# Optimization experiments

Measured on AMD Instinct MI355X. Metric: run time of the kernel, lower is better.

## Reference

```python
import jax, jax.numpy as jnp
import numpy as np

B, S, D = 1, 2048, 2048
H, KV = 32, 8
HD = D // H          # 64
R = H // KV          # 4 (GQA repeat factor)
ROPE_BASE = 10000.0


def setup_inputs() -> dict:
    key = jax.random.key(0)
    ks = jax.random.split(key, 5)
    x = jax.random.normal(ks[0], (B, S, D), jnp.float32)
    # Real rotary frequencies as (cos, sin) pairs: [S, HD//2, 2]
    inv_freq = 1.0 / (ROPE_BASE ** (np.arange(0, HD, 2, dtype=np.float64) / HD))
    ang = np.outer(np.arange(S, dtype=np.float64), inv_freq)
    freqs_cis = jnp.asarray(np.stack([np.cos(ang), np.sin(ang)], axis=-1), jnp.float32)
    std = 0.02
    wq = jax.random.normal(ks[1], (H * HD, D), jnp.float32) * std
    wk = jax.random.normal(ks[2], (KV * HD, D), jnp.float32) * std
    wv = jax.random.normal(ks[3], (KV * HD, D), jnp.float32) * std
    wo = jax.random.normal(ks[4], (D, H * HD), jnp.float32) * std
    return {"x": x, "freqs_cis": freqs_cis, "wq": wq, "wk": wk, "wv": wv, "wo": wo}


def _apply_rope(x, cos, sin):
    # x: [b, s, h, hd]; cos/sin: [s, hd//2]. Complex multiply on interleaved pairs.
    xr = x.reshape(*x.shape[:-1], HD // 2, 2)
    x0, x1 = xr[..., 0], xr[..., 1]
    c = cos[None, :, None, :]
    s = sin[None, :, None, :]
    o0 = x0 * c - x1 * s
    o1 = x0 * s + x1 * c
    return jnp.stack([o0, o1], axis=-1).reshape(x.shape)


def reference(x, freqs_cis, wq, wk, wv, wo):
    b, s, _ = x.shape
    q = (x @ wq.T).reshape(b, s, H, HD)
    k = (x @ wk.T).reshape(b, s, KV, HD)
    v = (x @ wv.T).reshape(b, s, KV, HD)
    cos, sin = freqs_cis[..., 0], freqs_cis[..., 1]
    q = _apply_rope(q, cos, sin)
    k = _apply_rope(k, cos, sin)
    # GQA: group q heads instead of repeat_interleave on k/v.
    # repeat_interleave maps kv-head g -> q heads [g*R, (g+1)*R), matching this reshape.
    qg = q.reshape(b, s, KV, R, HD)
    scale = 1.0 / np.sqrt(HD)
    scores = jnp.einsum('bsgrd,btgd->bgrst', qg, k) * scale  # [b, KV, R, s, t]
    causal = jnp.tril(jnp.ones((s, s), dtype=bool))
    scores = jnp.where(causal, scores, jnp.float32(-1e9))
    attn = jax.nn.softmax(scores.astype(jnp.float32), axis=-1).astype(q.dtype)
    out = jnp.einsum('bgrst,btgd->bsgrd', attn, v).reshape(b, s, H * HD)
    return out @ wo.T
```

## Files before the change

### kernel.cpp

```cpp
#include <hip/hip_runtime.h>

typedef unsigned short u16;
typedef unsigned int u32;
typedef __bf16 bf16x8 __attribute__((ext_vector_type(8)));
typedef unsigned short ushort8 __attribute__((ext_vector_type(8)));
typedef float floatx4 __attribute__((ext_vector_type(4)));
typedef u32 u32x2 __attribute__((ext_vector_type(2)));

#define S_LEN 2048
#define NH 32
#define NKV 8
#define HD_ 64
#define LDQ 3072

__device__ __forceinline__ u16 f2bf(float f) {
  unsigned u = __builtin_bit_cast(unsigned, f);
  u += 0x7FFF + ((u >> 16) & 1);
  return (u16)(u >> 16);
}
__device__ __forceinline__ float bf2f(u16 h) {
  unsigned u = ((unsigned)h) << 16;
  return __builtin_bit_cast(float, u);
}
__device__ __forceinline__ bf16x8 ld8(const u16* p) {
  return __builtin_bit_cast(bf16x8, *(const ushort8*)p);
}
__device__ __forceinline__ floatx4 mfma16(bf16x8 a, bf16x8 b, floatx4 c) {
  return __builtin_amdgcn_mfma_f32_16x16x32_bf16(a, b, c, 0, 0, 0);
}
__device__ __forceinline__ u32 pk2bf(float a, float b) {
  u32 ua = __builtin_bit_cast(u32, a) + 0x8000u;
  u32 ub = __builtin_bit_cast(u32, b) + 0x8000u;
  return __builtin_amdgcn_perm(ub, ua, 0x07060302);
}

__global__ void cvt_kernel(const float* __restrict__ in, u16* __restrict__ out, int n4) {
  int i = blockIdx.x * blockDim.x + threadIdx.x;
  if (i >= n4) return;
  float4 v = ((const float4*)in)[i];
  ((ushort4*)out)[i] = make_ushort4(f2bf(v.x), f2bf(v.y), f2bf(v.z), f2bf(v.w));
}

template <int TM, int TN, int OUT_BF16>
__global__ __launch_bounds__(256) void gemm_db(
    const u16* __restrict__ A, const u16* __restrict__ B, void* __restrict__ C,
    int ldc, int K, int lda) {
  __shared__ __align__(16) u16 As[2][TM * 64];
  __shared__ __align__(16) u16 Bs[2][TN * 64];
  const int tid = threadIdx.x;
  const int wave = tid >> 6, lane = tid & 63;
  const int quad = lane >> 4, l16 = lane & 15;
  const int bm = blockIdx.y * TM, bn = blockIdx.x * TN;
  const int wr = (wave >> 1) * (TM / 2), wc = (wave & 1) * (TN / 2);
  constexpr int MI = TM / 32, NI = TN / 32;
  const int crow = tid >> 3, col8 = tid & 7;

  size_t aoff[MI], boff[NI];
#pragma unroll
  for (int j = 0; j < MI; j++) aoff[j] = (size_t)(bm + crow + j * 32) * lda + col8 * 8;
#pragma unroll
  for (int j = 0; j < NI; j++) boff[j] = (size_t)(bn + crow + j * 32) * K + col8 * 8;

  ushort8 a8[MI], b8[NI];
  auto load_tiles = [&](int k0) {
#pragma unroll
    for (int j = 0; j < MI; j++) a8[j] = *(const ushort8*)(A + aoff[j] + k0);
#pragma unroll
    for (int j = 0; j < NI; j++) b8[j] = *(const ushort8*)(B + boff[j] + k0);
  };
  auto write_tiles = [&](int p) {
#pragma unroll
    for (int j = 0; j < MI; j++) {
      const int row = crow + j * 32;
      *(ushort8*)&As[p][row * 64 + ((col8 ^ (row & 7)) * 8)] = a8[j];
    }
#pragma unroll
    for (int j = 0; j < NI; j++) {
      const int row = crow + j * 32;
      *(ushort8*)&Bs[p][row * 64 + ((col8 ^ (row & 7)) * 8)] = b8[j];
    }
  };

  floatx4 acc[MI][NI] = {};
  load_tiles(0);
  write_tiles(0);
  __syncthreads();
  int p = 0;
  for (int k0 = 0; k0 < K; k0 += 64) {
    const bool more = (k0 + 64 < K);
    if (more) load_tiles(k0 + 64);
#pragma unroll
    for (int kh = 0; kh < 2; kh++) {
      bf16x8 af[MI], bfr[NI];
#pragma unroll
      for (int mi = 0; mi < MI; mi++) {
        const int row = wr + mi * 16 + l16;
        af[mi] = ld8(&As[p][row * 64 + (((kh * 4 + quad) ^ (row & 7)) * 8)]);
      }
#pragma unroll
      for (int ni = 0; ni < NI; ni++) {
        const int row = wc + ni * 16 + l16;
        bfr[ni] = ld8(&Bs[p][row * 64 + (((kh * 4 + quad) ^ (row & 7)) * 8)]);
      }
#pragma unroll
      for (int mi = 0; mi < MI; mi++)
#pragma unroll
        for (int ni = 0; ni < NI; ni++)
          acc[mi][ni] = mfma16(af[mi], bfr[ni], acc[mi][ni]);
    }
    if (more) {
      write_tiles(p ^ 1);
      __syncthreads();
      p ^= 1;
    }
  }

#pragma unroll
  for (int mi = 0; mi < MI; mi++)
#pragma unroll
    for (int ni = 0; ni < NI; ni++)
#pragma unroll
      for (int r = 0; r < 4; r++) {
        const int row = bm + wr + mi * 16 + quad * 4 + r;
        const int col = bn + wc + ni * 16 + l16;
        if (OUT_BF16) ((u16*)C)[(size_t)row * ldc + col] = f2bf(acc[mi][ni][r]);
        else          ((float*)C)[(size_t)row * ldc + col] = acc[mi][ni][r];
      }
}

__global__ void rope_kernel(u16* __restrict__ qk, const float* __restrict__ fc, int h_bits,
                            int row_stride, float scale) {
  int idx = blockIdx.x * blockDim.x + threadIdx.x;
  int d = idx & 31;
  int t = idx >> 5;
  int hh = t & ((1 << h_bits) - 1);
  int s = t >> h_bits;
  float c  = fc[s * 64 + d * 2];
  float sn = fc[s * 64 + d * 2 + 1];
  size_t base = (size_t)s * row_stride + hh * 64 + d * 2;
  float x0 = bf2f(qk[base]), x1 = bf2f(qk[base + 1]);
  qk[base]     = f2bf((x0 * c - x1 * sn) * scale);
  qk[base + 1] = f2bf((x0 * sn + x1 * c) * scale);
}

__global__ void transpose_v(const u16* __restrict__ qkv, u16* __restrict__ vT) {
  int idx = blockIdx.x * blockDim.x + threadIdx.x;
  int s = idx & (S_LEN - 1);
  int t = idx >> 11;
  vT[idx] = qkv[(size_t)s * LDQ + 2560 + t];
}

__global__ __launch_bounds__(256) void attn_kernel(const u16* qkv, const u16* __restrict__ vT,
                                                   u16* __restrict__ o) {
  __shared__ __align__(16) u16 Ks[64 * 72];
  __shared__ __align__(16) u16 Vs[64 * 72];
  __shared__ __align__(16) u16 pS[4][16 * 72];
  const int h = blockIdx.x;
  const int g = h >> 2;
  const int tid = threadIdx.x;
  const int wave = tid >> 6, lane = tid & 63;
  const int quad = lane >> 4, l16 = lane & 15;
  const int qtA = (int)blockIdx.y;
  const int qtB = 31 - qtA;

  const ushort8 ones_u = {0x3F80, 0x3F80, 0x3F80, 0x3F80, 0x3F80, 0x3F80, 0x3F80, 0x3F80};
  const bf16x8 onesA = __builtin_bit_cast(bf16x8, ones_u);

  const int qrow = wave * 16 + l16;
  const size_t qoffA = (size_t)(qtA * 64 + qrow) * LDQ + h * HD_;
  const size_t qoffB = (size_t)(qtB * 64 + qrow) * LDQ + h * HD_;
  bf16x8 qfA0 = ld8(qkv + qoffA + quad * 8);
  bf16x8 qfA1 = ld8(qkv + qoffA + 32 + quad * 8);
  bf16x8 qfB0 = ld8(qkv + qoffB + quad * 8);
  bf16x8 qfB1 = ld8(qkv + qoffB + 32 + quad * 8);

  const int r0 = tid >> 3,         o0 = (tid & 7) * 8;
  const int r1 = (tid + 256) >> 3, o1 = o0;
  const u16* ksrc = qkv + 2048 + g * HD_;
  const u16* vsrc = vT + (size_t)g * HD_ * S_LEN;

  ushort8 kp0 = *(const ushort8*)(ksrc + (size_t)r0 * LDQ + o0);
  ushort8 kp1 = *(const ushort8*)(ksrc + (size_t)r1 * LDQ + o1);
  ushort8 vp0 = *(const ushort8*)(vsrc + (size_t)r0 * S_LEN + o0);
  ushort8 vp1 = *(const ushort8*)(vsrc + (size_t)r1 * S_LEN + o1);

  u16* myP = &pS[wave][0];

  for (int ph = 0; ph < 2; ph++) {
    const int qt = ph ? qtB : qtA;
    const int qglob = qt * 64 + qrow;
    const bf16x8 qf0 = ph ? qfB0 : qfA0;
    const bf16x8 qf1 = ph ? qfB1 : qfA1;
    floatx4 Ofrag[4] = {};
    floatx4 lacc = {};

    for (int kt = 0; kt <= qt; kt++) {
      const int kbase = kt * 64;
      *(ushort8*)&Ks[r0 * 72 + o0] = kp0;
      *(ushort8*)&Ks[r1 * 72 + o1] = kp1;
      *(ushort8*)&Vs[r0 * 72 + o0] = vp0;
      *(ushort8*)&Vs[r1 * 72 + o1] = vp1;
      __syncthreads();
      const bool last = (kt == qt);
      if (!last || ph == 0) {
        const int nb = last ? 0 : kbase + 64;
        kp0 = *(const ushort8*)(ksrc + (size_t)(nb + r0) * LDQ + o0);
        kp1 = *(const ushort8*)(ksrc + (size_t)(nb + r1) * LDQ + o1);
        vp0 = *(const ushort8*)(vsrc + (size_t)r0 * S_LEN + nb + o0);
        vp1 = *(const ushort8*)(vsrc + (size_t)r1 * S_LEN + nb + o1);
      }
      floatx4 sf[4];
#pragma unroll
      for (int sub = 0; sub < 4; sub++) {
        const u16* kb = &Ks[(sub * 16 + l16) * 72];
        floatx4 s = {};
        s = mfma16(ld8(kb + quad * 8), qf0, s);
        s = mfma16(ld8(kb + 32 + quad * 8), qf1, s);
        sf[sub] = s;
      }
      if (last) {
#pragma unroll
        for (int sub = 0; sub < 4; sub++)
#pragma unroll
          for (int r = 0; r < 4; r++)
            if (kbase + sub * 16 + quad * 4 + r > qglob) sf[sub][r] = -INFINITY;
      }
      u32x2 pk[4];
#pragma unroll
      for (int sub = 0; sub < 4; sub++) {
        float p0 = __builtin_amdgcn_exp2f(sf[sub][0]);
        float p1 = __builtin_amdgcn_exp2f(sf[sub][1]);
        float p2 = __builtin_amdgcn_exp2f(sf[sub][2]);
        float p3 = __builtin_amdgcn_exp2f(sf[sub][3]);
        pk[sub].x = pk2bf(p0, p1);
        pk[sub].y = pk2bf(p2, p3);
      }
      bf16x8 vf[4][2];
#pragma unroll
      for (int nt = 0; nt < 4; nt++) {
        const u16* vb = &Vs[(nt * 16 + l16) * 72 + quad * 8];
        vf[nt][0] = ld8(vb);
        vf[nt][1] = ld8(vb + 32);
      }
#pragma unroll
      for (int sub = 0; sub < 4; sub++)
        *(u32x2*)&myP[l16 * 72 + sub * 16 + quad * 4] = pk[sub];
      asm volatile("s_waitcnt lgkmcnt(0)" ::: "memory");
      bf16x8 pf0 = ld8(&myP[l16 * 72 + quad * 8]);
      bf16x8 pf1 = ld8(&myP[l16 * 72 + 32 + quad * 8]);
#pragma unroll
      for (int nt = 0; nt < 4; nt++) {
        Ofrag[nt] = mfma16(vf[nt][0], pf0, Ofrag[nt]);
        Ofrag[nt] = mfma16(vf[nt][1], pf1, Ofrag[nt]);
      }
      lacc = mfma16(onesA, pf0, lacc);
      lacc = mfma16(onesA, pf1, lacc);
      __syncthreads();
    }

    const float inv = 1.0f / lacc[0];
    const size_t ooff = (size_t)qglob * 2048 + h * HD_;
#pragma unroll
    for (int nt = 0; nt < 4; nt++)
#pragma unroll
      for (int r = 0; r < 4; r++) {
        int hd = nt * 16 + quad * 4 + r;
        o[ooff + hd] = f2bf(Ofrag[nt][r] * inv);
      }
  }
}

extern "C" void kernel_launch(void* const* d_in, const int* in_sizes, int n_in,
                              void* d_out, int out_size, void* d_ws, size_t ws_size,
                              hipStream_t stream) {
  const float* x  = (const float*)d_in[0];
  const float* fc = (const float*)d_in[1];
  const float* wq = (const float*)d_in[2];
  const float* wk = (const float*)d_in[3];
  const float* wv = (const float*)d_in[4];
  const float* wo = (const float*)d_in[5];
  float* out = (float*)d_out;

  char* ws = (char*)d_ws;
  const size_t MB = 1024 * 1024;
  u16* qkv = (u16*)(ws);
  u16* wb  = (u16*)(ws + 12 * MB);
  u16* vTb = (u16*)(ws + 12 * MB);
  u16* wob = (u16*)(ws + 14 * MB);
  u16* ob  = (u16*)(ws + 22 * MB);
  u16* xb  = (u16*)d_out;
  (void)ws_size; (void)n_in; (void)in_sizes; (void)out_size;

  cvt_kernel<<<4096, 256, 0, stream>>>(x,  xb, 1048576);
  cvt_kernel<<<4096, 256, 0, stream>>>(wq, wb, 1048576);
  cvt_kernel<<<1024, 256, 0, stream>>>(wk, wb + (size_t)2048 * 2048, 262144);
  cvt_kernel<<<1024, 256, 0, stream>>>(wv, wb + (size_t)2560 * 2048, 262144);
  gemm_db<128, 96, 1><<<dim3(32, 16), 256, 0, stream>>>(xb, wb, qkv, LDQ, 2048, 2048);
  cvt_kernel<<<4096, 256, 0, stream>>>(wo, wob, 1048576);
  rope_kernel<<<8192, 256, 0, stream>>>(qkv, fc, 5, LDQ, 0.18033688f);
  rope_kernel<<<2048, 256, 0, stream>>>(qkv + 2048, fc, 3, LDQ, 1.0f);
  transpose_v<<<4096, 256, 0, stream>>>(qkv, vTb);
  attn_kernel<<<dim3(NH, 16), 256, 0, stream>>>(qkv, vTb, ob);
  gemm_db<128, 64, 0><<<dim3(32, 16), 256, 0, stream>>>(ob, wob, out, 2048, 2048, 2048);
}
```

Baseline: 233.8 us.

## Share K/V tiles across paired query tiles with double-buffered swizzled LDS

The attention kernel now processes its low and high causal query tiles together in one sweep over key tiles. Each K/V tile loaded into shared memory serves both query tiles, where before each of the two phases reloaded it. Shared memory is double-buffered, so the next tile is stored before compute and only one barrier runs per iteration. Row padding is replaced by an XOR swizzle. This cuts global and LDS traffic and synchronisation, at the cost of more registers for two sets of accumulators and divergent actA branches.

Result: no change. 231.8 us (-0.9%).

```diff
diff --git a/kernel.cpp b/kernel.cpp
--- a/kernel.cpp
+++ b/kernel.cpp
@@ -152,122 +152,176 @@
 
 __global__ __launch_bounds__(256) void attn_kernel(const u16* qkv, const u16* __restrict__ vT,
                                                    u16* __restrict__ o) {
-  __shared__ __align__(16) u16 Ks[64 * 72];
-  __shared__ __align__(16) u16 Vs[64 * 72];
-  __shared__ __align__(16) u16 pS[4][16 * 72];
+  __shared__ __align__(16) u16 Ks[2][64 * 64];
+  __shared__ __align__(16) u16 Vs[2][64 * 64];
+  __shared__ __align__(16) u16 pS[8][16 * 64];
   const int h = blockIdx.x;
   const int g = h >> 2;
   const int tid = threadIdx.x;
   const int wave = tid >> 6, lane = tid & 63;
   const int quad = lane >> 4, l16 = lane & 15;
-  const int qtA = (int)blockIdx.y;
-  const int qtB = 31 - qtA;
+  const int y = (int)blockIdx.y;
+  const int p_ = (y < 8) ? y : 23 - y;
+  const int qlo = p_, qhi = 31 - p_;
 
   const ushort8 ones_u = {0x3F80, 0x3F80, 0x3F80, 0x3F80, 0x3F80, 0x3F80, 0x3F80, 0x3F80};
   const bf16x8 onesA = __builtin_bit_cast(bf16x8, ones_u);
 
   const int qrow = wave * 16 + l16;
-  const size_t qoffA = (size_t)(qtA * 64 + qrow) * LDQ + h * HD_;
-  const size_t qoffB = (size_t)(qtB * 64 + qrow) * LDQ + h * HD_;
+  const int qgA = qlo * 64 + qrow, qgB = qhi * 64 + qrow;
+  const size_t qoffA = (size_t)qgA * LDQ + h * HD_;
+  const size_t qoffB = (size_t)qgB * LDQ + h * HD_;
   bf16x8 qfA0 = ld8(qkv + qoffA + quad * 8);
   bf16x8 qfA1 = ld8(qkv + qoffA + 32 + quad * 8);
   bf16x8 qfB0 = ld8(qkv + qoffB + quad * 8);
   bf16x8 qfB1 = ld8(qkv + qoffB + 32 + quad * 8);
 
-  const int r0 = tid >> 3,         o0 = (tid & 7) * 8;
-  const int r1 = (tid + 256) >> 3, o1 = o0;
+  const int r0 = tid >> 3, r1 = r0 + 32;
+  const int col8 = tid & 7;
+  const int so = (col8 ^ (r0 & 7)) * 8;
+  const int o0 = col8 * 8;
   const u16* ksrc = qkv + 2048 + g * HD_;
   const u16* vsrc = vT + (size_t)g * HD_ * S_LEN;
 
   ushort8 kp0 = *(const ushort8*)(ksrc + (size_t)r0 * LDQ + o0);
-  ushort8 kp1 = *(const ushort8*)(ksrc + (size_t)r1 * LDQ + o1);
+  ushort8 kp1 = *(const ushort8*)(ksrc + (size_t)r1 * LDQ + o0);
   ushort8 vp0 = *(const ushort8*)(vsrc + (size_t)r0 * S_LEN + o0);
-  ushort8 vp1 = *(const ushort8*)(vsrc + (size_t)r1 * S_LEN + o1);
-
-  u16* myP = &pS[wave][0];
-
-  for (int ph = 0; ph < 2; ph++) {
-    const int qt = ph ? qtB : qtA;
-    const int qglob = qt * 64 + qrow;
-    const bf16x8 qf0 = ph ? qfB0 : qfA0;
-    const bf16x8 qf1 = ph ? qfB1 : qfA1;
-    floatx4 Ofrag[4] = {};
-    floatx4 lacc = {};
-
-    for (int kt = 0; kt <= qt; kt++) {
-      const int kbase = kt * 64;
-      *(ushort8*)&Ks[r0 * 72 + o0] = kp0;
-      *(ushort8*)&Ks[r1 * 72 + o1] = kp1;
-      *(ushort8*)&Vs[r0 * 72 + o0] = vp0;
-      *(ushort8*)&Vs[r1 * 72 + o1] = vp1;
+  ushort8 vp1 = *(const ushort8*)(vsrc + (size_t)r1 * S_LEN + o0);
+
+  floatx4 OA[4] = {}, OB[4] = {};
+  floatx4 lA = {}, lB = {};
+  u16* myPA = &pS[wave][0];
+  u16* myPB = &pS[wave + 4][0];
+
+  *(ushort8*)&Ks[0][r0 * 64 + so] = kp0;
+  *(ushort8*)&Ks[0][r1 * 64 + so] = kp1;
+  *(ushort8*)&Vs[0][r0 * 64 + so] = vp0;
+  *(ushort8*)&Vs[0][r1 * 64 + so] = vp1;
+  kp0 = *(const ushort8*)(ksrc + (size_t)(64 + r0) * LDQ + o0);
+  kp1 = *(const ushort8*)(ksrc + (size_t)(64 + r1) * LDQ + o0);
+  vp0 = *(const ushort8*)(vsrc + (size_t)r0 * S_LEN + 64 + o0);
+  vp1 = *(const ushort8*)(vsrc + (size_t)r1 * S_LEN + 64 + o0);
+  __syncthreads();
+  int pp = 0;
+
+  for (int kt = 0; kt <= qhi; kt++) {
+    const int kbase = kt * 64;
+    const bool more = kt < qhi;
+    if (more) {
+      *(ushort8*)&Ks[pp ^ 1][r0 * 64 + so] = kp0;
+      *(ushort8*)&Ks[pp ^ 1][r1 * 64 + so] = kp1;
+      *(ushort8*)&Vs[pp ^ 1][r0 * 64 + so] = vp0;
+      *(ushort8*)&Vs[pp ^ 1][r1 * 64 + so] = vp1;
+      if (kt + 1 < qhi) {
+        const int nb = kbase + 128;
+        kp0 = *(const ushort8*)(ksrc + (size_t)(nb + r0) * LDQ + o0);
+        kp1 = *(const ushort8*)(ksrc + (size_t)(nb + r1) * LDQ + o0);
+        vp0 = *(const ushort8*)(vsrc + (size_t)r0 * S_LEN + nb + o0);
+        vp1 = *(const ushort8*)(vsrc + (size_t)r1 * S_LEN + nb + o0);
+      }
+    }
+    const u16* Kc = &Ks[pp][0];
+    const u16* Vc = &Vs[pp][0];
+    const bool actA = (kt <= qlo);
+
+    floatx4 sfA[4], sfB[4];
+#pragma unroll
+    for (int sub = 0; sub < 4; sub++) {
+      const int row = sub * 16 + l16;
+      const u16* kb = Kc + row * 64;
+      bf16x8 k0 = ld8(kb + ((quad ^ (l16 & 7)) * 8));
+      bf16x8 k1 = ld8(kb + (((4 + quad) ^ (l16 & 7)) * 8));
+      floatx4 sB = {};
+      sB = mfma16(k0, qfB0, sB);
+      sB = mfma16(k1, qfB1, sB);
+      sfB[sub] = sB;
+      if (actA) {
+        floatx4 sA = {};
+        sA = mfma16(k0, qfA0, sA);
+        sA = mfma16(k1, qfA1, sA);
+        sfA[sub] = sA;
+      }
+    }
+    if (kt == qhi) {
+#pragma unroll
+      for (int sub = 0; sub < 4; sub++)
+#pragma unroll
+        for (int r = 0; r < 4; r++)
+          if (kbase + sub * 16 + quad * 4 + r > qgB) sfB[sub][r] = -INFINITY;
+    }
+    if (kt == qlo) {
+#pragma unroll
+      for (int sub = 0; sub < 4; sub++)
+#pragma unroll
+        for (int r = 0; r < 4; r++)
+          if (kbase + sub * 16 + quad * 4 + r > qgA) sfA[sub][r] = -INFINITY;
+    }
+
+    u32x2 pkA[4], pkB[4];
+#pragma unroll
+    for (int sub = 0; sub < 4; sub++) {
+      pkB[sub].x = pk2bf(__builtin_amdgcn_exp2f(sfB[sub][0]), __builtin_amdgcn_exp2f(sfB[sub][1]));
+      pkB[sub].y = pk2bf(__builtin_amdgcn_exp2f(sfB[sub][2]), __builtin_amdgcn_exp2f(sfB[sub][3]));
+      if (actA) {
+        pkA[sub].x = pk2bf(__builtin_amdgcn_exp2f(sfA[sub][0]), __builtin_amdgcn_exp2f(sfA[sub][1]));
+        pkA[sub].y = pk2bf(__builtin_amdgcn_exp2f(sfA[sub][2]), __builtin_amdgcn_exp2f(sfA[sub][3]));
+      }
+    }
+
+    bf16x8 vf[4][2];
+#pragma unroll
+    for (int nt = 0; nt < 4; nt++) {
+      const u16* vb = Vc + (nt * 16 + l16) * 64;
+      vf[nt][0] = ld8(vb + ((quad ^ (l16 & 7)) * 8));
+      vf[nt][1] = ld8(vb + (((4 + quad) ^ (l16 & 7)) * 8));
+    }
+
+#pragma unroll
+    for (int sub = 0; sub < 4; sub++) {
+      const int slot = (2 * sub + (quad >> 1)) ^ (l16 & 7);
+      const int a = l16 * 64 + slot * 8 + (quad & 1) * 4;
+      *(u32x2*)&myPB[a] = pkB[sub];
+      if (actA) *(u32x2*)&myPA[a] = pkA[sub];
+    }
+    asm volatile("s_waitcnt lgkmcnt(0)" ::: "memory");
+    bf16x8 pB0 = ld8(&myPB[l16 * 64 + ((quad ^ (l16 & 7)) * 8)]);
+    bf16x8 pB1 = ld8(&myPB[l16 * 64 + (((4 + quad) ^ (l16 & 7)) * 8)]);
+#pragma unroll
+    for (int nt = 0; nt < 4; nt++) {
+      OB[nt] = mfma16(vf[nt][0], pB0, OB[nt]);
+      OB[nt] = mfma16(vf[nt][1], pB1, OB[nt]);
+    }
+    lB = mfma16(onesA, pB0, lB);
+    lB = mfma16(onesA, pB1, lB);
+    if (actA) {
+      bf16x8 pA0 = ld8(&myPA[l16 * 64 + ((quad ^ (l16 & 7)) * 8)]);
+      bf16x8 pA1 = ld8(&myPA[l16 * 64 + (((4 + quad) ^ (l16 & 7)) * 8)]);
+#pragma unroll
+      for (int nt = 0; nt < 4; nt++) {
+        OA[nt] = mfma16(vf[nt][0], pA0, OA[nt]);
+        OA[nt] = mfma16(vf[nt][1], pA1, OA[nt]);
+      }
+      lA = mfma16(onesA, pA0, lA);
+      lA = mfma16(onesA, pA1, lA);
+    }
+    if (more) {
       __syncthreads();
-      const bool last = (kt == qt);
-      if (!last || ph == 0) {
-        const int nb = last ? 0 : kbase + 64;
-        kp0 = *(const ushort8*)(ksrc + (size_t)(nb + r0) * LDQ + o0);
-        kp1 = *(const ushort8*)(ksrc + (size_t)(nb + r1) * LDQ + o1);
-        vp0 = *(const ushort8*)(vsrc + (size_t)r0 * S_LEN + nb + o0);
-        vp1 = *(const ushort8*)(vsrc + (size_t)r1 * S_LEN + nb + o1);
-      }
-      floatx4 sf[4];
-#pragma unroll
-      for (int sub = 0; sub < 4; sub++) {
-        const u16* kb = &Ks[(sub * 16 + l16) * 72];
-        floatx4 s = {};
-        s = mfma16(ld8(kb + quad * 8), qf0, s);
-        s = mfma16(ld8(kb + 32 + quad * 8), qf1, s);
-        sf[sub] = s;
-      }
-      if (last) {
-#pragma unroll
-        for (int sub = 0; sub < 4; sub++)
-#pragma unroll
-          for (int r = 0; r < 4; r++)
-            if (kbase + sub * 16 + quad * 4 + r > qglob) sf[sub][r] = -INFINITY;
-      }
-      u32x2 pk[4];
-#pragma unroll
-      for (int sub = 0; sub < 4; sub++) {
-        float p0 = __builtin_amdgcn_exp2f(sf[sub][0]);
-        float p1 = __builtin_amdgcn_exp2f(sf[sub][1]);
-        float p2 = __builtin_amdgcn_exp2f(sf[sub][2]);
-        float p3 = __builtin_amdgcn_exp2f(sf[sub][3]);
-        pk[sub].x = pk2bf(p0, p1);
-        pk[sub].y = pk2bf(p2, p3);
-      }
-      bf16x8 vf[4][2];
-#pragma unroll
-      for (int nt = 0; nt < 4; nt++) {
-        const u16* vb = &Vs[(nt * 16 + l16) * 72 + quad * 8];
-        vf[nt][0] = ld8(vb);
-        vf[nt][1] = ld8(vb + 32);
-      }
-#pragma unroll
-      for (int sub = 0; sub < 4; sub++)
-        *(u32x2*)&myP[l16 * 72 + sub * 16 + quad * 4] = pk[sub];
-      asm volatile("s_waitcnt lgkmcnt(0)" ::: "memory");
-      bf16x8 pf0 = ld8(&myP[l16 * 72 + quad * 8]);
-      bf16x8 pf1 = ld8(&myP[l16 * 72 + 32 + quad * 8]);
-#pragma unroll
-      for (int nt = 0; nt < 4; nt++) {
-        Ofrag[nt] = mfma16(vf[nt][0], pf0, Ofrag[nt]);
-        Ofrag[nt] = mfma16(vf[nt][1], pf1, Ofrag[nt]);
-      }
-      lacc = mfma16(onesA, pf0, lacc);
-      lacc = mfma16(onesA, pf1, lacc);
-      __syncthreads();
-    }
-
-    const float inv = 1.0f / lacc[0];
-    const size_t ooff = (size_t)qglob * 2048 + h * HD_;
-#pragma unroll
-    for (int nt = 0; nt < 4; nt++)
-#pragma unroll
-      for (int r = 0; r < 4; r++) {
-        int hd = nt * 16 + quad * 4 + r;
-        o[ooff + hd] = f2bf(Ofrag[nt][r] * inv);
-      }
+      pp ^= 1;
+    }
   }
+
+  const float invA = 1.0f / lA[0];
+  const float invB = 1.0f / lB[0];
+  const size_t ooffA = (size_t)qgA * 2048 + h * HD_;
+  const size_t ooffB = (size_t)qgB * 2048 + h * HD_;
+#pragma unroll
+  for (int nt = 0; nt < 4; nt++)
+#pragma unroll
+    for (int r = 0; r < 4; r++) {
+      const int hd = nt * 16 + quad * 4 + r;
+      o[ooffA + hd] = f2bf(OA[nt][r] * invA);
+      o[ooffB + hd] = f2bf(OB[nt][r] * invB);
+    }
 }
 
 extern "C" void kernel_launch(void* const* d_in, const int* in_sizes, int n_in,
```
